# Kernel optimization log

Hardware: AMD Instinct MI355X
Metric: run time of the kernel (lower is better)

Reference implementation:

```python
import jax, jax.numpy as jnp
import numpy as np

N_NODES = 50000
N_EDGES = 800000
IN_CH = 128
HID = 64
OUT_CH = 64
N_CLASSES = 10
N_GRAPHS = 256


def setup_inputs() -> dict:
    key = jax.random.key(0)
    ks = jax.random.split(key, 10)
    x = jax.random.normal(ks[0], (N_NODES, IN_CH), dtype=jnp.float32)
    edge_index = jax.random.randint(ks[1], (2, N_EDGES), 0, N_NODES, dtype=jnp.int32)
    edge_attr = jax.random.normal(ks[2], (N_EDGES, 16), dtype=jnp.float32)
    batch = jnp.sort(jax.random.randint(ks[3], (N_NODES,), 0, N_GRAPHS, dtype=jnp.int32))
    # learned parameters (Glorot-ish scale)
    W1 = jax.random.normal(ks[4], (IN_CH, HID), dtype=jnp.float32) / np.sqrt(IN_CH)
    b1 = jnp.zeros((HID,), dtype=jnp.float32)
    W2 = jax.random.normal(ks[5], (HID, OUT_CH), dtype=jnp.float32) / np.sqrt(HID)
    b2 = jnp.zeros((OUT_CH,), dtype=jnp.float32)
    Wl = jax.random.normal(ks[6], (OUT_CH, N_CLASSES), dtype=jnp.float32) / np.sqrt(OUT_CH)
    bl = jnp.zeros((N_CLASSES,), dtype=jnp.float32)
    return {"x": x, "edge_index": edge_index, "edge_attr": edge_attr, "batch": batch,
            "W1": W1, "b1": b1, "W2": W2, "b2": b2, "Wl": Wl, "bl": bl}


def _gcn_layer(h_in, W, b, src, dst, dinv):
    """Standard GCNConv: D^{-1/2}(A+I)D^{-1/2} X W + b (self-loops included)."""
    h = h_in @ W                                   # [N, F_out]
    norm = (dinv[src] * dinv[dst])[:, None]        # [E, 1]
    msg = h[src] * norm                            # gather + scale
    agg = jax.ops.segment_sum(msg, dst, num_segments=N_NODES)  # scatter-add
    agg = agg + h * (dinv * dinv)[:, None]         # self-loop contribution
    return agg + b


def reference(x, edge_index, edge_attr, batch, W1, b1, W2, b2, Wl, bl):
    src, dst = edge_index[0], edge_index[1]
    # symmetric normalization degrees with self-loops
    deg = jax.ops.segment_sum(jnp.ones((N_EDGES,), x.dtype), dst,
                              num_segments=N_NODES) + 1.0
    dinv = jax.lax.rsqrt(deg)
    h = jax.nn.relu(_gcn_layer(x, W1, b1, src, dst, dinv))
    h = _gcn_layer(h, W2, b2, src, dst, dinv)
    # global_mean_pool over graph ids
    counts = jax.ops.segment_sum(jnp.ones((N_NODES,), x.dtype), batch,
                                 num_segments=N_GRAPHS)
    pooled = jax.ops.segment_sum(h, batch, num_segments=N_GRAPHS)
    pooled = pooled / jnp.maximum(counts, 1.0)[:, None]
    # dropout is identity in eval mode
    return pooled @ Wl + bl                        # [N_GRAPHS, N_CLASSES]
```

## Files before the change

kernel.cpp:

```cpp
#include <hip/hip_runtime.h>

#define N_NODES   50000
#define N_EDGES   800000
#define IN_CH     128
#define HID       64
#define OUT_CH    64
#define N_CLASSES 10
#define N_GRAPHS  256

__global__ __launch_bounds__(256) void deg_kernel(const int* __restrict__ ei,
                                                  int* __restrict__ cnt) {
    int e = blockIdx.x * 256 + threadIdx.x;
    if (e >= N_EDGES) return;
    atomicAdd(&cnt[ei[N_EDGES + e]], 1);
}

__global__ __launch_bounds__(256) void scan1_kernel(const int* __restrict__ cnt,
                                                    int* __restrict__ excl,
                                                    int* __restrict__ part) {
    __shared__ int s[256];
    int t = threadIdx.x, i = blockIdx.x * 256 + t;
    int v = (i < N_NODES) ? cnt[i] : 0;
    s[t] = v; __syncthreads();
    for (int off = 1; off < 256; off <<= 1) {
        int x = (t >= off) ? s[t - off] : 0;
        __syncthreads();
        s[t] += x;
        __syncthreads();
    }
    if (i < N_NODES) excl[i] = s[t] - v;
    if (t == 255) part[blockIdx.x] = s[t];
}

__global__ __launch_bounds__(256) void scan2_kernel(int* __restrict__ part,
                                                    int nblk) {
    __shared__ int s[256];
    int t = threadIdx.x;
    int v = (t < nblk) ? part[t] : 0;
    s[t] = v; __syncthreads();
    for (int off = 1; off < 256; off <<= 1) {
        int x = (t >= off) ? s[t - off] : 0;
        __syncthreads();
        s[t] += x;
        __syncthreads();
    }
    if (t < nblk) part[t] = s[t] - v;
}

__global__ __launch_bounds__(256) void scan3_kernel(const int* __restrict__ excl,
                                                    const int* __restrict__ part,
                                                    const int* __restrict__ cnt,
                                                    int* __restrict__ rs,
                                                    int* __restrict__ cur,
                                                    float* __restrict__ dinv) {
    int i = blockIdx.x * 256 + threadIdx.x;
    if (i >= N_NODES) {
        if (i == N_NODES) rs[N_NODES] = N_EDGES;
        return;
    }
    int v = excl[i] + part[blockIdx.x];
    rs[i] = v;
    cur[i] = v;
    dinv[i] = rsqrtf((float)cnt[i] + 1.0f);
}

__global__ __launch_bounds__(256) void bucket_kernel(const int* __restrict__ ei,
                                                     const float* __restrict__ dinv,
                                                     int* __restrict__ cur,
                                                     int2* __restrict__ pack) {
    int e = blockIdx.x * 256 + threadIdx.x;
    if (e >= N_EDGES) return;
    int s = ei[e];
    int d = ei[N_EDGES + e];
    float norm = dinv[s] * dinv[d];
    int pos = atomicAdd(&cur[d], 1);
    pack[pos] = make_int2(s, __float_as_int(norm));
}

template <int K, bool RELU>
__global__ __launch_bounds__(256) void gemm_kernel(
    const float* __restrict__ X, const float* __restrict__ W,
    const float* __restrict__ b, const float* __restrict__ dinv,
    float* __restrict__ hout, float* __restrict__ agg) {
    __shared__ float xs[16][K + 1];
    __shared__ float ws[K][64];
    const int tid = threadIdx.x;
    const int base = blockIdx.x * 16;

    for (int i = tid; i < K * 64; i += 256) (&ws[0][0])[i] = W[i];
    for (int i = tid; i < 16 * K; i += 256) {
        int r = i / K, k = i % K;
        int n = base + r;
        float v = (n < N_NODES) ? X[n * K + k] : 0.0f;
        if (RELU) v = fmaxf(v, 0.0f);
        xs[r][k] = v;
    }
    __syncthreads();

    const int sub = tid >> 4;
    const int c0  = (tid & 15) * 4;
    const int n   = base + sub;
    float a0 = 0.f, a1 = 0.f, a2 = 0.f, a3 = 0.f;
#pragma unroll 16
    for (int k = 0; k < K; ++k) {
        float xv  = xs[sub][k];
        float4 wv = *reinterpret_cast<const float4*>(&ws[k][c0]);
        a0 += xv * wv.x; a1 += xv * wv.y; a2 += xv * wv.z; a3 += xv * wv.w;
    }
    if (n < N_NODES) {
        float di = dinv[n];
        float dd = di * di;
        float4 bb = *reinterpret_cast<const float4*>(&b[c0]);
        *reinterpret_cast<float4*>(&hout[n * 64 + c0]) =
            make_float4(a0, a1, a2, a3);
        *reinterpret_cast<float4*>(&agg[n * 64 + c0]) =
            make_float4(a0 * dd + bb.x, a1 * dd + bb.y,
                        a2 * dd + bb.z, a3 * dd + bb.w);
    }
}

__global__ __launch_bounds__(256) void gather_kernel(const int* __restrict__ rs,
                                                     const int2* __restrict__ pack,
                                                     const float* __restrict__ h,
                                                     float* __restrict__ agg) {
    int n = blockIdx.x * 4 + (threadIdx.x >> 6);
    if (n >= N_NODES) return;
    int lane = threadIdx.x & 63;
    int e   = rs[n];
    int end = rs[n + 1];
    float acc = agg[n * 64 + lane];
    for (; e + 3 < end; e += 4) {
        int2 p0 = pack[e];
        int2 p1 = pack[e + 1];
        int2 p2 = pack[e + 2];
        int2 p3 = pack[e + 3];
        float h0 = h[(size_t)p0.x * 64 + lane];
        float h1 = h[(size_t)p1.x * 64 + lane];
        float h2 = h[(size_t)p2.x * 64 + lane];
        float h3 = h[(size_t)p3.x * 64 + lane];
        acc += __int_as_float(p0.y) * h0;
        acc += __int_as_float(p1.y) * h1;
        acc += __int_as_float(p2.y) * h2;
        acc += __int_as_float(p3.y) * h3;
    }
    for (; e < end; ++e) {
        int2 p = pack[e];
        acc += __int_as_float(p.y) * h[(size_t)p.x * 64 + lane];
    }
    agg[n * 64 + lane] = acc;
}

__global__ __launch_bounds__(256) void pool_kernel(const int* __restrict__ batch,
                                                   const float* __restrict__ h2,
                                                   float* __restrict__ pooled) {
    int wave = threadIdx.x >> 6;
    int lane = threadIdx.x & 63;
    int base = blockIdx.x * 256 + wave * 64;
    if (base >= N_NODES) return;
    int endn = base + 64;
    if (endn > N_NODES) endn = N_NODES;
    int curg = batch[base];
    float acc = 0.0f;
    for (int n = base; n < endn; ++n) {
        int g = batch[n];
        if (g != curg) {
            atomicAdd(&pooled[curg * 64 + lane], acc);
            acc = 0.0f;
            curg = g;
        }
        acc += h2[(size_t)n * 64 + lane];
    }
    atomicAdd(&pooled[curg * 64 + lane], acc);
}

__global__ __launch_bounds__(256) void bound_kernel(const int* __restrict__ batch,
                                                    int* __restrict__ start) {
    int n = blockIdx.x * 256 + threadIdx.x;
    if (n >= N_NODES) return;
    int cur  = batch[n];
    int prev = (n == 0) ? -1 : batch[n - 1];
    for (int g = prev + 1; g <= cur; ++g) start[g] = n;
    if (n == N_NODES - 1)
        for (int g = cur + 1; g <= N_GRAPHS; ++g) start[g] = N_NODES;
}

__global__ __launch_bounds__(256) void head_kernel(const float* __restrict__ pooled,
                                                   const int* __restrict__ start,
                                                   const float* __restrict__ Wl,
                                                   const float* __restrict__ bl,
                                                   float* __restrict__ out) {
    int gid = blockIdx.x * 256 + threadIdx.x;
    if (gid >= N_GRAPHS * N_CLASSES) return;
    int g = gid / N_CLASSES, c = gid % N_CLASSES;
    float cntf = (float)(start[g + 1] - start[g]);
    float inv = 1.0f / fmaxf(cntf, 1.0f);
    float acc = 0.f;
#pragma unroll
    for (int k = 0; k < OUT_CH; ++k)
        acc += pooled[g * 64 + k] * Wl[k * N_CLASSES + c];
    out[gid] = acc * inv + bl[c];
}

extern "C" void kernel_launch(void* const* d_in, const int* in_sizes, int n_in,
                              void* d_out, int out_size, void* d_ws, size_t ws_size,
                              hipStream_t stream) {
    const float* x     = (const float*)d_in[0];
    const int*   ei    = (const int*)d_in[1];
    const int*   batch = (const int*)d_in[3];
    const float* W1    = (const float*)d_in[4];
    const float* b1    = (const float*)d_in[5];
    const float* W2    = (const float*)d_in[6];
    const float* b2    = (const float*)d_in[7];
    const float* Wl    = (const float*)d_in[8];
    const float* bl    = (const float*)d_in[9];
    float* out = (float*)d_out;

    int*   wsI    = (int*)d_ws;
    int*   cnt    = wsI;
    float* pooled = (float*)(wsI + 50048);
    int*   start  = wsI + 66432;
    float* dinv   = (float*)(wsI + 66689 + 63);
    int*   excl   = wsI + 116800;
    int*   part   = wsI + 166848;
    int*   rs     = wsI + 167104;
    int*   cur    = wsI + 217168;
    int2*  pack   = (int2*)(wsI + 267216);
    float* hA     = (float*)(wsI + 1867216);
    float* aggB   = (float*)(wsI + 5067216);

    const int NBLK = (N_NODES + 255) / 256;

    hipMemsetAsync(wsI, 0, (size_t)66432 * sizeof(int), stream);

    deg_kernel  <<<(N_EDGES + 255) / 256, 256, 0, stream>>>(ei, cnt);
    scan1_kernel<<<NBLK, 256, 0, stream>>>(cnt, excl, part);
    scan2_kernel<<<1, 256, 0, stream>>>(part, NBLK);
    scan3_kernel<<<NBLK + 1, 256, 0, stream>>>(excl, part, cnt, rs, cur, dinv);
    bucket_kernel<<<(N_EDGES + 255) / 256, 256, 0, stream>>>(ei, dinv, cur, pack);

    gemm_kernel<IN_CH, false><<<(N_NODES + 15) / 16, 256, 0, stream>>>(
        x, W1, b1, dinv, hA, aggB);
    gather_kernel<<<(N_NODES + 3) / 4, 256, 0, stream>>>(rs, pack, hA, aggB);

    gemm_kernel<HID, true><<<(N_NODES + 15) / 16, 256, 0, stream>>>(
        aggB, W2, b2, dinv, hA, aggB);
    gather_kernel<<<(N_NODES + 3) / 4, 256, 0, stream>>>(rs, pack, hA, aggB);

    pool_kernel <<<NBLK, 256, 0, stream>>>(batch, aggB, pooled);
    bound_kernel<<<NBLK, 256, 0, stream>>>(batch, start);
    head_kernel <<<(N_GRAPHS * N_CLASSES + 255) / 256, 256, 0, stream>>>(
        pooled, start, Wl, bl, out);
}
```

Before: 371.1 us.

## Prescale features by dinv, drop per-edge norms, fuse gather with GEMM and pooling

New measurement: 357.0 us. 1.04x faster.

```diff
diff --git a/kernel.cpp b/kernel.cpp
--- a/kernel.cpp
+++ b/kernel.cpp
@@ -65,35 +65,28 @@
 }
 
 __global__ __launch_bounds__(256) void bucket_kernel(const int* __restrict__ ei,
-                                                     const float* __restrict__ dinv,
                                                      int* __restrict__ cur,
-                                                     int2* __restrict__ pack) {
+                                                     int* __restrict__ pack) {
     int e = blockIdx.x * 256 + threadIdx.x;
     if (e >= N_EDGES) return;
     int s = ei[e];
     int d = ei[N_EDGES + e];
-    float norm = dinv[s] * dinv[d];
     int pos = atomicAdd(&cur[d], 1);
-    pack[pos] = make_int2(s, __float_as_int(norm));
-}
-
-template <int K, bool RELU>
-__global__ __launch_bounds__(256) void gemm_kernel(
+    pack[pos] = s;
+}
+
+__global__ __launch_bounds__(256) void gemm1_kernel(
     const float* __restrict__ X, const float* __restrict__ W,
-    const float* __restrict__ b, const float* __restrict__ dinv,
-    float* __restrict__ hout, float* __restrict__ agg) {
-    __shared__ float xs[16][K + 1];
-    __shared__ float ws[K][64];
+    const float* __restrict__ dinv, float* __restrict__ hs) {
+    __shared__ float xs[16][IN_CH + 1];
+    __shared__ float ws[IN_CH][64];
     const int tid = threadIdx.x;
     const int base = blockIdx.x * 16;
 
-    for (int i = tid; i < K * 64; i += 256) (&ws[0][0])[i] = W[i];
-    for (int i = tid; i < 16 * K; i += 256) {
-        int r = i / K, k = i % K;
-        int n = base + r;
-        float v = (n < N_NODES) ? X[n * K + k] : 0.0f;
-        if (RELU) v = fmaxf(v, 0.0f);
-        xs[r][k] = v;
+    for (int i = tid; i < IN_CH * 64; i += 256) (&ws[0][0])[i] = W[i];
+    for (int i = tid; i < 16 * IN_CH; i += 256) {
+        int r = i / IN_CH, k = i % IN_CH;
+        xs[r][k] = X[(size_t)(base + r) * IN_CH + k];
     }
     __syncthreads();
 
@@ -102,75 +95,105 @@
     const int n   = base + sub;
     float a0 = 0.f, a1 = 0.f, a2 = 0.f, a3 = 0.f;
 #pragma unroll 16
-    for (int k = 0; k < K; ++k) {
+    for (int k = 0; k < IN_CH; ++k) {
         float xv  = xs[sub][k];
         float4 wv = *reinterpret_cast<const float4*>(&ws[k][c0]);
         a0 += xv * wv.x; a1 += xv * wv.y; a2 += xv * wv.z; a3 += xv * wv.w;
     }
-    if (n < N_NODES) {
-        float di = dinv[n];
-        float dd = di * di;
-        float4 bb = *reinterpret_cast<const float4*>(&b[c0]);
-        *reinterpret_cast<float4*>(&hout[n * 64 + c0]) =
-            make_float4(a0, a1, a2, a3);
-        *reinterpret_cast<float4*>(&agg[n * 64 + c0]) =
-            make_float4(a0 * dd + bb.x, a1 * dd + bb.y,
-                        a2 * dd + bb.z, a3 * dd + bb.w);
-    }
-}
-
-__global__ __launch_bounds__(256) void gather_kernel(const int* __restrict__ rs,
-                                                     const int2* __restrict__ pack,
-                                                     const float* __restrict__ h,
-                                                     float* __restrict__ agg) {
-    int n = blockIdx.x * 4 + (threadIdx.x >> 6);
-    if (n >= N_NODES) return;
-    int lane = threadIdx.x & 63;
-    int e   = rs[n];
-    int end = rs[n + 1];
-    float acc = agg[n * 64 + lane];
-    for (; e + 3 < end; e += 4) {
-        int2 p0 = pack[e];
-        int2 p1 = pack[e + 1];
-        int2 p2 = pack[e + 2];
-        int2 p3 = pack[e + 3];
-        float h0 = h[(size_t)p0.x * 64 + lane];
-        float h1 = h[(size_t)p1.x * 64 + lane];
-        float h2 = h[(size_t)p2.x * 64 + lane];
-        float h3 = h[(size_t)p3.x * 64 + lane];
-        acc += __int_as_float(p0.y) * h0;
-        acc += __int_as_float(p1.y) * h1;
-        acc += __int_as_float(p2.y) * h2;
-        acc += __int_as_float(p3.y) * h3;
-    }
-    for (; e < end; ++e) {
-        int2 p = pack[e];
-        acc += __int_as_float(p.y) * h[(size_t)p.x * 64 + lane];
-    }
-    agg[n * 64 + lane] = acc;
-}
-
-__global__ __launch_bounds__(256) void pool_kernel(const int* __restrict__ batch,
-                                                   const float* __restrict__ h2,
-                                                   float* __restrict__ pooled) {
+    float di = dinv[n];
+    *reinterpret_cast<float4*>(&hs[(size_t)n * 64 + c0]) =
+        make_float4(a0 * di, a1 * di, a2 * di, a3 * di);
+}
+
+__global__ __launch_bounds__(256) void gemmgather2_kernel(
+    const int* __restrict__ rs, const int* __restrict__ pack,
+    const float* __restrict__ hs1, const float* __restrict__ dinv,
+    const float* __restrict__ W2, const float* __restrict__ b1,
+    float* __restrict__ hs2) {
+    __shared__ float xs[16][64];
+    __shared__ float ws[64][64];
+    const int tid  = threadIdx.x;
+    const int base = blockIdx.x * 16;
+    const int wave = tid >> 6;
+    const int lane = tid & 63;
+
+    for (int i = tid; i < 64 * 64; i += 256) (&ws[0][0])[i] = W2[i];
+
+    const float bb = b1[lane];
+    for (int r = wave * 4; r < wave * 4 + 4; ++r) {
+        int n = base + r;
+        float own = hs1[(size_t)n * 64 + lane];
+        float di  = dinv[n];
+        int e = rs[n], end = rs[n + 1];
+        float acc = 0.f;
+        for (; e + 3 < end; e += 4) {
+            int s0 = pack[e], s1 = pack[e + 1], s2 = pack[e + 2], s3 = pack[e + 3];
+            float h0 = hs1[(size_t)s0 * 64 + lane];
+            float h1 = hs1[(size_t)s1 * 64 + lane];
+            float h2 = hs1[(size_t)s2 * 64 + lane];
+            float h3 = hs1[(size_t)s3 * 64 + lane];
+            acc += h0 + h1 + h2 + h3;
+        }
+        for (; e < end; ++e)
+            acc += hs1[(size_t)pack[e] * 64 + lane];
+        xs[r][lane] = fmaxf(di * (own + acc) + bb, 0.f);
+    }
+    __syncthreads();
+
+    const int sub = tid >> 4;
+    const int c0  = (tid & 15) * 4;
+    const int n   = base + sub;
+    float a0 = 0.f, a1 = 0.f, a2 = 0.f, a3 = 0.f;
+#pragma unroll 16
+    for (int k = 0; k < 64; ++k) {
+        float xv  = xs[sub][k];
+        float4 wv = *reinterpret_cast<const float4*>(&ws[k][c0]);
+        a0 += xv * wv.x; a1 += xv * wv.y; a2 += xv * wv.z; a3 += xv * wv.w;
+    }
+    float di = dinv[n];
+    *reinterpret_cast<float4*>(&hs2[(size_t)n * 64 + c0]) =
+        make_float4(a0 * di, a1 * di, a2 * di, a3 * di);
+}
+
+__global__ __launch_bounds__(256) void gatherpool_kernel(
+    const int* __restrict__ rs, const int* __restrict__ pack,
+    const float* __restrict__ hs2, const float* __restrict__ dinv,
+    const float* __restrict__ b2, const int* __restrict__ batch,
+    float* __restrict__ pooled) {
     int wave = threadIdx.x >> 6;
     int lane = threadIdx.x & 63;
-    int base = blockIdx.x * 256 + wave * 64;
+    int base = blockIdx.x * 64 + wave * 16;
     if (base >= N_NODES) return;
-    int endn = base + 64;
+    int endn = base + 16;
     if (endn > N_NODES) endn = N_NODES;
+    const float bb = b2[lane];
     int curg = batch[base];
-    float acc = 0.0f;
+    float racc = 0.f;
     for (int n = base; n < endn; ++n) {
+        float own = hs2[(size_t)n * 64 + lane];
+        float di  = dinv[n];
+        int e = rs[n], end = rs[n + 1];
+        float acc = 0.f;
+        for (; e + 3 < end; e += 4) {
+            int s0 = pack[e], s1 = pack[e + 1], s2 = pack[e + 2], s3 = pack[e + 3];
+            float h0 = hs2[(size_t)s0 * 64 + lane];
+            float h1 = hs2[(size_t)s1 * 64 + lane];
+            float h2 = hs2[(size_t)s2 * 64 + lane];
+            float h3 = hs2[(size_t)s3 * 64 + lane];
+            acc += h0 + h1 + h2 + h3;
+        }
+        for (; e < end; ++e)
+            acc += hs2[(size_t)pack[e] * 64 + lane];
+        float val = di * (own + acc) + bb;
         int g = batch[n];
         if (g != curg) {
-            atomicAdd(&pooled[curg * 64 + lane], acc);
-            acc = 0.0f;
+            atomicAdd(&pooled[curg * 64 + lane], racc);
+            racc = 0.f;
             curg = g;
         }
-        acc += h2[(size_t)n * 64 + lane];
-    }
-    atomicAdd(&pooled[curg * 64 + lane], acc);
+        racc += val;
+    }
+    atomicAdd(&pooled[curg * 64 + lane], racc);
 }
 
 __global__ __launch_bounds__(256) void bound_kernel(const int* __restrict__ batch,
@@ -219,34 +242,33 @@
     int*   cnt    = wsI;
     float* pooled = (float*)(wsI + 50048);
     int*   start  = wsI + 66432;
-    float* dinv   = (float*)(wsI + 66689 + 63);
+    float* dinv   = (float*)(wsI + 66752);
     int*   excl   = wsI + 116800;
     int*   part   = wsI + 166848;
     int*   rs     = wsI + 167104;
     int*   cur    = wsI + 217168;
-    int2*  pack   = (int2*)(wsI + 267216);
-    float* hA     = (float*)(wsI + 1867216);
-    float* aggB   = (float*)(wsI + 5067216);
+    int*   pack   = wsI + 267216;
+    float* hs1    = (float*)(wsI + 1067216);
+    float* hs2    = (float*)(wsI + 4267216);
 
     const int NBLK = (N_NODES + 255) / 256;
 
     hipMemsetAsync(wsI, 0, (size_t)66432 * sizeof(int), stream);
 
-    deg_kernel  <<<(N_EDGES + 255) / 256, 256, 0, stream>>>(ei, cnt);
-    scan1_kernel<<<NBLK, 256, 0, stream>>>(cnt, excl, part);
-    scan2_kernel<<<1, 256, 0, stream>>>(part, NBLK);
-    scan3_kernel<<<NBLK + 1, 256, 0, stream>>>(excl, part, cnt, rs, cur, dinv);
-    bucket_kernel<<<(N_EDGES + 255) / 256, 256, 0, stream>>>(ei, dinv, cur, pack);
-
-    gemm_kernel<IN_CH, false><<<(N_NODES + 15) / 16, 256, 0, stream>>>(
-        x, W1, b1, dinv, hA, aggB);
-    gather_kernel<<<(N_NODES + 3) / 4, 256, 0, stream>>>(rs, pack, hA, aggB);
-
-    gemm_kernel<HID, true><<<(N_NODES + 15) / 16, 256, 0, stream>>>(
-        aggB, W2, b2, dinv, hA, aggB);
-    gather_kernel<<<(N_NODES + 3) / 4, 256, 0, stream>>>(rs, pack, hA, aggB);
-
-    pool_kernel <<<NBLK, 256, 0, stream>>>(batch, aggB, pooled);
+    deg_kernel   <<<(N_EDGES + 255) / 256, 256, 0, stream>>>(ei, cnt);
+    scan1_kernel <<<NBLK, 256, 0, stream>>>(cnt, excl, part);
+    scan2_kernel <<<1, 256, 0, stream>>>(part, NBLK);
+    scan3_kernel <<<NBLK + 1, 256, 0, stream>>>(excl, part, cnt, rs, cur, dinv);
+    bucket_kernel<<<(N_EDGES + 255) / 256, 256, 0, stream>>>(ei, cur, pack);
+
+    gemm1_kernel<<<N_NODES / 16, 256, 0, stream>>>(x, W1, dinv, hs1);
+
+    gemmgather2_kernel<<<N_NODES / 16, 256, 0, stream>>>(
+        rs, pack, hs1, dinv, W2, b1, hs2);
+
+    gatherpool_kernel<<<(N_NODES + 63) / 64, 256, 0, stream>>>(
+        rs, pack, hs2, dinv, b2, batch, pooled);
+
     bound_kernel<<<NBLK, 256, 0, stream>>>(batch, start);
     head_kernel <<<(N_GRAPHS * N_CLASSES + 255) / 256, 256, 0, stream>>>(
         pooled, start, Wl, bl, out);
```
